# Kernel tuning notes

Hardware: AMD Instinct MI355X
Metric: run time of the kernel (lower is better)

## Reference

```python
import jax, jax.numpy as jnp
import numpy as np

B, L, D, H = 2, 2048, 1024, 16
HD = D // H


def _xavier(key, out_f, in_f):
    std = (2.0 / (in_f + out_f)) ** 0.5
    return jax.random.normal(key, (out_f, in_f), dtype=jnp.float32) * std


def setup_inputs() -> dict:
    key = jax.random.key(0)
    k = jax.random.split(key, 8)
    Q = jax.random.normal(k[0], (B, L, D), dtype=jnp.float32)
    K = jax.random.normal(k[1], (B, L, D), dtype=jnp.float32)
    V = jax.random.normal(k[2], (B, L, D), dtype=jnp.float32)
    mask = jnp.tril(jnp.ones((L, L), dtype=jnp.int32))[None, None]  # causal [1,1,L,L]
    wq = _xavier(k[3], D, D)
    wk = _xavier(k[4], D, D)
    wv = _xavier(k[5], D, D)
    wo = _xavier(k[6], D, D)
    bo = jnp.zeros((D,), dtype=jnp.float32)
    return {"Q": Q, "K": K, "V": V, "mask": mask,
            "wq": wq, "wk": wk, "wv": wv, "wo": wo, "bo": bo}


def reference(Q, K, V, mask, wq, wk, wv, wo, bo):
    N, Lq, Dm = Q.shape
    # projections: X @ W^T (Linear stores [out, in])
    q = (Q @ wq.T).reshape(N, Lq, H, HD).transpose(0, 2, 1, 3)  # [N,H,L,hd]
    kk = (K @ wk.T).reshape(N, Lq, H, HD).transpose(0, 2, 1, 3)
    v = (V @ wv.T).reshape(N, Lq, H, HD).transpose(0, 2, 1, 3)
    score = jnp.einsum('bhqd,bhkd->bhqk', q, kk) / jnp.sqrt(jnp.float32(HD))
    score = jnp.where(mask == 0, -jnp.inf, score)
    weights = jax.nn.softmax(score, axis=-1)
    attn = jnp.einsum('bhqk,bhkd->bhqd', weights, v)
    out = attn.transpose(0, 2, 1, 3).reshape(N, Lq, Dm)
    return out @ wo.T + bo
```

## Files before the change

kernel.cpp:

```cpp
#include <hip/hip_runtime.h>
#include <hip/hip_bf16.h>


#define B_ 2
#define L_ 2048
#define D_ 1024
#define H_ 16
#define HD_ 64
#define NA_ ((size_t)B_ * L_ * D_)
#define NW_ ((size_t)D_ * D_)

typedef __attribute__((ext_vector_type(8))) short bf16x8;
typedef __attribute__((ext_vector_type(4))) float f32x4;
typedef __hip_bfloat16 bf16;

__device__ __forceinline__ void async_load16(const void* g, void* l) {
  __builtin_amdgcn_global_load_lds((const __attribute__((address_space(1))) void*)g,
                                   (__attribute__((address_space(3))) void*)l,
                                   16, 0, 0);
}

__global__ __launch_bounds__(256) void xcvt_kernel(const float* __restrict__ q,
                                                   const float* __restrict__ k,
                                                   const float* __restrict__ v,
                                                   const float* __restrict__ w0,
                                                   const float* __restrict__ w1,
                                                   const float* __restrict__ w2,
                                                   const float* __restrict__ w3,
                                                   bf16* __restrict__ dst) {
  const int y = blockIdx.y;
  size_t i = ((size_t)blockIdx.x * 256 + threadIdx.x) * 4;
  const float* src;
  size_t soff = i;
  if (y < 3) {
    src = (y == 0) ? q : (y == 1) ? k : v;
  } else {
    int w = (int)(i >> 20);
    src = (w == 0) ? w0 : (w == 1) ? w1 : (w == 2) ? w2 : w3;
    soff = i & (NW_ - 1);
  }
  float4 vv = *(const float4*)(src + soff);
  union { bf16 h[4]; uint2 u; } pk;
  pk.h[0] = __float2bfloat16(vv.x);
  pk.h[1] = __float2bfloat16(vv.y);
  pk.h[2] = __float2bfloat16(vv.z);
  pk.h[3] = __float2bfloat16(vv.w);
  *(uint2*)(dst + (size_t)y * NA_ + i) = pk.u;
}

#define TS_ 136
__global__ __launch_bounds__(256) void gemm_qkv(const bf16* __restrict__ Qb,
                                                const bf16* __restrict__ Kb,
                                                const bf16* __restrict__ Vb,
                                                const bf16* __restrict__ Wb,
                                                bf16* __restrict__ qp,
                                                bf16* __restrict__ kp,
                                                bf16* __restrict__ vtp) {
  __shared__ __align__(16) bf16 smem[128 * TS_];
  bf16* As = smem;
  bf16* Bs = smem + 128 * 32;
  const int tid = threadIdx.x;
  const int wv = tid >> 6, lane = tid & 63;
  const int quad = lane >> 4, l16 = lane & 15;
  const int wm = wv & 1, wn = wv >> 1;
  const int m0 = blockIdx.x * 128, n0 = blockIdx.y * 128;
  const int z = blockIdx.z;
  const bf16* X = (z == 0) ? Qb : (z == 1) ? Kb : Vb;
  const bf16* W = Wb + (size_t)z * NW_;

  f32x4 acc[4][4];
#pragma unroll
  for (int i = 0; i < 4; i++)
#pragma unroll
    for (int j = 0; j < 4; j++) acc[i][j] = (f32x4){0.f, 0.f, 0.f, 0.f};

  for (int k0 = 0; k0 < D_; k0 += 32) {
#pragma unroll
    for (int it = 0; it < 2; it++) {
      int c = (wv * 2 + it) * 64 + lane;
      int row = c >> 2, cc = c & 3;
      async_load16(X + (size_t)(m0 + row) * D_ + k0 + cc * 8, (char*)As + c * 16);
      async_load16(W + (size_t)(n0 + row) * D_ + k0 + cc * 8, (char*)Bs + c * 16);
    }
    __syncthreads();
    bf16x8 af[4], bfr[4];
#pragma unroll
    for (int mi = 0; mi < 4; mi++)
      af[mi] = *(const bf16x8*)&As[(wm * 64 + mi * 16 + l16) * 32 + quad * 8];
#pragma unroll
    for (int ni = 0; ni < 4; ni++)
      bfr[ni] = *(const bf16x8*)&Bs[(wn * 64 + ni * 16 + l16) * 32 + quad * 8];
#pragma unroll
    for (int mi = 0; mi < 4; mi++)
#pragma unroll
      for (int ni = 0; ni < 4; ni++)
        acc[mi][ni] = __builtin_amdgcn_mfma_f32_16x16x32_bf16(af[mi], bfr[ni],
                                                              acc[mi][ni], 0, 0, 0);
    __syncthreads();
  }

  if (z == 2) {
    bf16* T = smem;
#pragma unroll
    for (int mi = 0; mi < 4; mi++) {
#pragma unroll
      for (int ni = 0; ni < 4; ni++) {
        int n_loc = wn * 64 + ni * 16 + l16;
        int m_loc = wm * 64 + mi * 16 + quad * 4;
        union { bf16 hx[4]; uint2 d; } pk;
#pragma unroll
        for (int r = 0; r < 4; r++) pk.hx[r] = __float2bfloat16(acc[mi][ni][r]);
        *(uint2*)&T[n_loc * TS_ + m_loc] = pk.d;
      }
    }
    __syncthreads();
#pragma unroll
    for (int p = 0; p < 8; p++) {
      int n_loc = p * 16 + (tid >> 4);
      int m_loc = (tid & 15) * 8;
      bf16x8 vv = *(const bf16x8*)&T[n_loc * TS_ + m_loc];
      int n = n0 + n_loc;
      int m = m0 + m_loc;
      int bb = m >> 11, l = m & (L_ - 1);
      int hh = n >> 6, hd = n & 63;
      *(bf16x8*)&vtp[((size_t)((bb * H_ + hh) * HD_ + hd)) * L_ + l] = vv;
    }
  } else {
    const float sc = (z == 0) ? 0.125f : 1.0f;
    bf16* dst = (z == 0) ? qp : kp;
#pragma unroll
    for (int mi = 0; mi < 4; mi++) {
#pragma unroll
      for (int ni = 0; ni < 4; ni++) {
        int n = n0 + wn * 64 + ni * 16 + l16;
#pragma unroll
        for (int r = 0; r < 4; r++) {
          int m = m0 + wm * 64 + mi * 16 + quad * 4 + r;
          dst[(size_t)m * D_ + n] = __float2bfloat16(acc[mi][ni][r] * sc);
        }
      }
    }
  }
}

__global__ __launch_bounds__(256) void attn_kernel(const bf16* __restrict__ qp,
                                                   const bf16* __restrict__ kp,
                                                   const bf16* __restrict__ vt,
                                                   bf16* __restrict__ attn) {
  __shared__ __align__(16) bf16 Kt[2][64 * 64];
  __shared__ __align__(16) bf16 Vt[2][64 * 64];
  __shared__ __align__(16) bf16 Pl[4][16 * 72];
  __shared__ __align__(16) bf16 Ph[4][16 * 72];
  const int tid = threadIdx.x;
  const int wv = tid >> 6, lane = tid & 63;
  const int quad = lane >> 4, l16 = lane & 15;
  const int pair = blockIdx.x, h = blockIdx.y, b = blockIdx.z;
  const int qlo = pair, qhi = (L_ / 64 - 1) - pair;

  const int rL = qlo * 64 + wv * 16 + l16;
  const int rH = qhi * 64 + wv * 16 + l16;
  bf16x8 qaL[2], qaH[2];
#pragma unroll
  for (int kk = 0; kk < 2; kk++) {
    qaL[kk] = *(const bf16x8*)&qp[((size_t)(b * L_ + rL)) * D_ + h * HD_ +
                                  kk * 32 + quad * 8];
    qaH[kk] = *(const bf16x8*)&qp[((size_t)(b * L_ + rH)) * D_ + h * HD_ +
                                  kk * 32 + quad * 8];
  }

  f32x4 OL[4], OH[4];
#pragma unroll
  for (int t = 0; t < 4; t++) {
    OL[t] = (f32x4){0.f, 0.f, 0.f, 0.f};
    OH[t] = (f32x4){0.f, 0.f, 0.f, 0.f};
  }
  float lL[4] = {0.f, 0.f, 0.f, 0.f}, lH[4] = {0.f, 0.f, 0.f, 0.f};

  const int csw = quad ^ (l16 & 7);

  auto stage = [&](int j, int buf) {
    const int j0 = j * 64;
#pragma unroll
    for (int it = 0; it < 2; it++) {
      int slot = (wv * 2 + it) * 64 + lane;
      int row = slot >> 3, c = (slot & 7) ^ (row & 7);
      async_load16(kp + ((size_t)(b * L_ + j0 + row)) * D_ + h * HD_ + c * 8,
                   (char*)Kt[buf] + slot * 16);
      async_load16(vt + ((size_t)((b * H_ + h) * HD_ + row)) * L_ + j0 + c * 8,
                   (char*)Vt[buf] + slot * 16);
    }
  };

  stage(0, 0);
  for (int j = 0; j <= qhi; j++) {
    const int buf = j & 1;
    const int j0 = j * 64;
    const bool doLo = (j <= qlo);
    __syncthreads();
    if (j < qhi) stage(j + 1, buf ^ 1);

    f32x4 sL[4], sH[4];
#pragma unroll
    for (int ss = 0; ss < 4; ss++) {
      int krow = ss * 16 + l16;
      bf16x8 kb0 = *(const bf16x8*)&Kt[buf][krow * 64 + csw * 8];
      bf16x8 kb1 = *(const bf16x8*)&Kt[buf][krow * 64 + (csw ^ 4) * 8];
      f32x4 s = (f32x4){0.f, 0.f, 0.f, 0.f};
      s = __builtin_amdgcn_mfma_f32_16x16x32_bf16(qaH[0], kb0, s, 0, 0, 0);
      s = __builtin_amdgcn_mfma_f32_16x16x32_bf16(qaH[1], kb1, s, 0, 0, 0);
      sH[ss] = s;
      if (doLo) {
        f32x4 t = (f32x4){0.f, 0.f, 0.f, 0.f};
        t = __builtin_amdgcn_mfma_f32_16x16x32_bf16(qaL[0], kb0, t, 0, 0, 0);
        t = __builtin_amdgcn_mfma_f32_16x16x32_bf16(qaL[1], kb1, t, 0, 0, 0);
        sL[ss] = t;
      }
    }

    if (j == qhi) {
#pragma unroll
      for (int ss = 0; ss < 4; ss++) {
        int key = j0 + ss * 16 + l16;
#pragma unroll
        for (int r = 0; r < 4; r++) {
          int rq = qhi * 64 + wv * 16 + quad * 4 + r;
          if (key > rq) sH[ss][r] = -1e30f;
        }
      }
    }
    if (doLo && j == qlo) {
#pragma unroll
      for (int ss = 0; ss < 4; ss++) {
        int key = j0 + ss * 16 + l16;
#pragma unroll
        for (int r = 0; r < 4; r++) {
          int rq = qlo * 64 + wv * 16 + quad * 4 + r;
          if (key > rq) sL[ss][r] = -1e30f;
        }
      }
    }
#pragma unroll
    for (int ss = 0; ss < 4; ss++) {
#pragma unroll
      for (int r = 0; r < 4; r++) {
        float p = __expf(sH[ss][r]);
        lH[r] += p;
        Ph[wv][(quad * 4 + r) * 72 + ss * 16 + l16] = __float2bfloat16(p);
      }
    }
    if (doLo) {
#pragma unroll
      for (int ss = 0; ss < 4; ss++) {
#pragma unroll
        for (int r = 0; r < 4; r++) {
          float p = __expf(sL[ss][r]);
          lL[r] += p;
          Pl[wv][(quad * 4 + r) * 72 + ss * 16 + l16] = __float2bfloat16(p);
        }
      }
    }

    asm volatile("s_waitcnt lgkmcnt(0)" ::: "memory");

#pragma unroll
    for (int kk = 0; kk < 2; kk++) {
      bf16x8 pah = *(const bf16x8*)&Ph[wv][l16 * 72 + kk * 32 + quad * 8];
      bf16x8 pal;
      if (doLo) pal = *(const bf16x8*)&Pl[wv][l16 * 72 + kk * 32 + quad * 8];
#pragma unroll
      for (int t = 0; t < 4; t++) {
        bf16x8 vb = *(const bf16x8*)&Vt[buf][(t * 16 + l16) * 64 + (csw ^ (kk * 4)) * 8];
        OH[t] = __builtin_amdgcn_mfma_f32_16x16x32_bf16(pah, vb, OH[t], 0, 0, 0);
        if (doLo) OL[t] = __builtin_amdgcn_mfma_f32_16x16x32_bf16(pal, vb, OL[t], 0, 0, 0);
      }
    }
  }

#pragma unroll
  for (int r = 0; r < 4; r++) {
#pragma unroll
    for (int off = 1; off < 16; off <<= 1) {
      lL[r] += __shfl_xor(lL[r], off, 64);
      lH[r] += __shfl_xor(lH[r], off, 64);
    }
  }
#pragma unroll
  for (int t = 0; t < 4; t++) {
#pragma unroll
    for (int r = 0; r < 4; r++) {
      int rowL = qlo * 64 + wv * 16 + quad * 4 + r;
      int rowH = qhi * 64 + wv * 16 + quad * 4 + r;
      attn[((size_t)(b * L_ + rowL)) * D_ + h * HD_ + t * 16 + l16] =
          __float2bfloat16(OL[t][r] / lL[r]);
      attn[((size_t)(b * L_ + rowH)) * D_ + h * HD_ + t * 16 + l16] =
          __float2bfloat16(OH[t][r] / lH[r]);
    }
  }
}

__global__ __launch_bounds__(256) void gemm_out(const bf16* __restrict__ X,
                                                const bf16* __restrict__ W,
                                                const float* __restrict__ bias,
                                                float* __restrict__ out) {
  __shared__ __align__(16) bf16 As[64 * 32];
  __shared__ __align__(16) bf16 Bs[128 * 32];
  const int tid = threadIdx.x;
  const int wv = tid >> 6, lane = tid & 63;
  const int quad = lane >> 4, l16 = lane & 15;
  const int wm = wv & 1, wn = wv >> 1;
  const int m0 = blockIdx.x * 64, n0 = blockIdx.y * 128;

  f32x4 acc[2][4];
#pragma unroll
  for (int i = 0; i < 2; i++)
#pragma unroll
    for (int j = 0; j < 4; j++) acc[i][j] = (f32x4){0.f, 0.f, 0.f, 0.f};

  for (int k0 = 0; k0 < D_; k0 += 32) {
    {
      int c = tid;
      int row = c >> 2, cc = c & 3;
      async_load16(X + (size_t)(m0 + row) * D_ + k0 + cc * 8, (char*)As + c * 16);
    }
#pragma unroll
    for (int it = 0; it < 2; it++) {
      int c = (wv * 2 + it) * 64 + lane;
      int row = c >> 2, cc = c & 3;
      async_load16(W + (size_t)(n0 + row) * D_ + k0 + cc * 8, (char*)Bs + c * 16);
    }
    __syncthreads();
    bf16x8 af[2], bfr[4];
#pragma unroll
    for (int mi = 0; mi < 2; mi++)
      af[mi] = *(const bf16x8*)&As[(wm * 32 + mi * 16 + l16) * 32 + quad * 8];
#pragma unroll
    for (int ni = 0; ni < 4; ni++)
      bfr[ni] = *(const bf16x8*)&Bs[(wn * 64 + ni * 16 + l16) * 32 + quad * 8];
#pragma unroll
    for (int mi = 0; mi < 2; mi++)
#pragma unroll
      for (int ni = 0; ni < 4; ni++)
        acc[mi][ni] = __builtin_amdgcn_mfma_f32_16x16x32_bf16(af[mi], bfr[ni],
                                                              acc[mi][ni], 0, 0, 0);
    __syncthreads();
  }

#pragma unroll
  for (int mi = 0; mi < 2; mi++) {
#pragma unroll
    for (int ni = 0; ni < 4; ni++) {
      int n = n0 + wn * 64 + ni * 16 + l16;
      float bval = bias[n];
#pragma unroll
      for (int r = 0; r < 4; r++) {
        int m = m0 + wm * 32 + mi * 16 + quad * 4 + r;
        out[(size_t)m * D_ + n] = acc[mi][ni][r] + bval;
      }
    }
  }
}

extern "C" void kernel_launch(void* const* d_in, const int* in_sizes, int n_in,
                              void* d_out, int out_size, void* d_ws, size_t ws_size,
                              hipStream_t stream) {
  const float* Q  = (const float*)d_in[0];
  const float* K  = (const float*)d_in[1];
  const float* V  = (const float*)d_in[2];
  const float* wq = (const float*)d_in[4];
  const float* wk = (const float*)d_in[5];
  const float* wvp = (const float*)d_in[6];
  const float* wo = (const float*)d_in[7];
  const float* bo = (const float*)d_in[8];
  float* out = (float*)d_out;

  bf16* base = (bf16*)d_ws;
  bf16* Qb = base;
  bf16* Kb = Qb + NA_;
  bf16* Vb = Kb + NA_;
  bf16* Wb = Vb + NA_;
  bf16* qp = Wb + 4 * NW_;
  bf16* kp = qp + NA_;
  bf16* vt = kp + NA_;
  bf16* at = vt + NA_;

  xcvt_kernel<<<dim3(NA_ / 1024, 4), 256, 0, stream>>>(Q, K, V, wq, wk, wvp, wo, base);
  gemm_qkv<<<dim3(32, 8, 3), 256, 0, stream>>>(Qb, Kb, Vb, Wb, qp, kp, vt);
  attn_kernel<<<dim3(L_ / 128, H_, B_), 256, 0, stream>>>(qp, kp, vt, at);
  gemm_out<<<dim3(64, 8), 256, 0, stream>>>(at, Wb + 3 * NW_, bo, out);
}
```

Baseline: 232.1 us.

## Swizzle GEMM block order per XCD and transpose attention score MFMA layout

Both GEMM kernels remap the linear block id so that consecutive ids sent round-robin to the 8 XCDs handle neighbouring tiles, improving L2 reuse of the A/B panels. In the attention kernel the score MFMA operands are swapped, so each lane holds 4 consecutive keys for a single query row. This lets P be written to LDS as one packed 8-byte store instead of four scalar bf16 stores, and the row sum becomes one scalar per lane, cutting the end-of-kernel shuffle reduction. s_setprio is raised around the MFMA phases to favour matrix issue across waves. The changes risk subtle mask and indexing mistakes, and the remap assumes exact grid sizes.

```diff
diff --git a/kernel.cpp b/kernel.cpp
--- a/kernel.cpp
+++ b/kernel.cpp
@@ -63,8 +63,10 @@
   const int wv = tid >> 6, lane = tid & 63;
   const int quad = lane >> 4, l16 = lane & 15;
   const int wm = wv & 1, wn = wv >> 1;
-  const int m0 = blockIdx.x * 128, n0 = blockIdx.y * 128;
-  const int z = blockIdx.z;
+  const int id = blockIdx.x + 32 * blockIdx.y + 256 * blockIdx.z;
+  const int swz = (id & 7) * 96 + (id >> 3);
+  const int m0 = (swz & 31) * 128, n0 = ((swz >> 5) & 7) * 128;
+  const int z = swz >> 8;
   const bf16* X = (z == 0) ? Qb : (z == 1) ? Kb : Vb;
   const bf16* W = Wb + (size_t)z * NW_;
 
@@ -157,14 +159,14 @@
   const int pair = blockIdx.x, h = blockIdx.y, b = blockIdx.z;
   const int qlo = pair, qhi = (L_ / 64 - 1) - pair;
 
-  const int rL = qlo * 64 + wv * 16 + l16;
-  const int rH = qhi * 64 + wv * 16 + l16;
+  const int rLq = qlo * 64 + wv * 16 + l16;
+  const int rHq = qhi * 64 + wv * 16 + l16;
   bf16x8 qaL[2], qaH[2];
 #pragma unroll
   for (int kk = 0; kk < 2; kk++) {
-    qaL[kk] = *(const bf16x8*)&qp[((size_t)(b * L_ + rL)) * D_ + h * HD_ +
+    qaL[kk] = *(const bf16x8*)&qp[((size_t)(b * L_ + rLq)) * D_ + h * HD_ +
                                   kk * 32 + quad * 8];
-    qaH[kk] = *(const bf16x8*)&qp[((size_t)(b * L_ + rH)) * D_ + h * HD_ +
+    qaH[kk] = *(const bf16x8*)&qp[((size_t)(b * L_ + rHq)) * D_ + h * HD_ +
                                   kk * 32 + quad * 8];
   }
 
@@ -174,7 +176,7 @@
     OL[t] = (f32x4){0.f, 0.f, 0.f, 0.f};
     OH[t] = (f32x4){0.f, 0.f, 0.f, 0.f};
   }
-  float lL[4] = {0.f, 0.f, 0.f, 0.f}, lH[4] = {0.f, 0.f, 0.f, 0.f};
+  float lL = 0.f, lH = 0.f;
 
   const int csw = quad ^ (l16 & 7);
 
@@ -200,68 +202,74 @@
     if (j < qhi) stage(j + 1, buf ^ 1);
 
     f32x4 sL[4], sH[4];
+    __builtin_amdgcn_s_setprio(1);
 #pragma unroll
     for (int ss = 0; ss < 4; ss++) {
       int krow = ss * 16 + l16;
       bf16x8 kb0 = *(const bf16x8*)&Kt[buf][krow * 64 + csw * 8];
       bf16x8 kb1 = *(const bf16x8*)&Kt[buf][krow * 64 + (csw ^ 4) * 8];
-      f32x4 s = (f32x4){0.f, 0.f, 0.f, 0.f};
-      s = __builtin_amdgcn_mfma_f32_16x16x32_bf16(qaH[0], kb0, s, 0, 0, 0);
-      s = __builtin_amdgcn_mfma_f32_16x16x32_bf16(qaH[1], kb1, s, 0, 0, 0);
-      sH[ss] = s;
+      f32x4 t = (f32x4){0.f, 0.f, 0.f, 0.f};
+      t = __builtin_amdgcn_mfma_f32_16x16x32_bf16(kb0, qaH[0], t, 0, 0, 0);
+      t = __builtin_amdgcn_mfma_f32_16x16x32_bf16(kb1, qaH[1], t, 0, 0, 0);
+      sH[ss] = t;
       if (doLo) {
-        f32x4 t = (f32x4){0.f, 0.f, 0.f, 0.f};
-        t = __builtin_amdgcn_mfma_f32_16x16x32_bf16(qaL[0], kb0, t, 0, 0, 0);
-        t = __builtin_amdgcn_mfma_f32_16x16x32_bf16(qaL[1], kb1, t, 0, 0, 0);
-        sL[ss] = t;
-      }
-    }
+        f32x4 u = (f32x4){0.f, 0.f, 0.f, 0.f};
+        u = __builtin_amdgcn_mfma_f32_16x16x32_bf16(kb0, qaL[0], u, 0, 0, 0);
+        u = __builtin_amdgcn_mfma_f32_16x16x32_bf16(kb1, qaL[1], u, 0, 0, 0);
+        sL[ss] = u;
+      }
+    }
+    __builtin_amdgcn_s_setprio(0);
 
     if (j == qhi) {
 #pragma unroll
+      for (int ss = 0; ss < 4; ss++)
+#pragma unroll
+        for (int r = 0; r < 4; r++) {
+          int key = j0 + ss * 16 + quad * 4 + r;
+          if (key > rHq) sH[ss][r] = -1e30f;
+        }
+    }
+    if (doLo && j == qlo) {
+#pragma unroll
+      for (int ss = 0; ss < 4; ss++)
+#pragma unroll
+        for (int r = 0; r < 4; r++) {
+          int key = j0 + ss * 16 + quad * 4 + r;
+          if (key > rLq) sL[ss][r] = -1e30f;
+        }
+    }
+
+#pragma unroll
+    for (int ss = 0; ss < 4; ss++) {
+      float p0 = __expf(sH[ss][0]), p1 = __expf(sH[ss][1]);
+      float p2 = __expf(sH[ss][2]), p3 = __expf(sH[ss][3]);
+      lH += (p0 + p1) + (p2 + p3);
+      union { bf16 hx[4]; uint2 d; } pk;
+      pk.hx[0] = __float2bfloat16(p0);
+      pk.hx[1] = __float2bfloat16(p1);
+      pk.hx[2] = __float2bfloat16(p2);
+      pk.hx[3] = __float2bfloat16(p3);
+      *(uint2*)&Ph[wv][l16 * 72 + ss * 16 + quad * 4] = pk.d;
+    }
+    if (doLo) {
+#pragma unroll
       for (int ss = 0; ss < 4; ss++) {
-        int key = j0 + ss * 16 + l16;
-#pragma unroll
-        for (int r = 0; r < 4; r++) {
-          int rq = qhi * 64 + wv * 16 + quad * 4 + r;
-          if (key > rq) sH[ss][r] = -1e30f;
-        }
-      }
-    }
-    if (doLo && j == qlo) {
-#pragma unroll
-      for (int ss = 0; ss < 4; ss++) {
-        int key = j0 + ss * 16 + l16;
-#pragma unroll
-        for (int r = 0; r < 4; r++) {
-          int rq = qlo * 64 + wv * 16 + quad * 4 + r;
-          if (key > rq) sL[ss][r] = -1e30f;
-        }
-      }
-    }
-#pragma unroll
-    for (int ss = 0; ss < 4; ss++) {
-#pragma unroll
-      for (int r = 0; r < 4; r++) {
-        float p = __expf(sH[ss][r]);
-        lH[r] += p;
-        Ph[wv][(quad * 4 + r) * 72 + ss * 16 + l16] = __float2bfloat16(p);
-      }
-    }
-    if (doLo) {
-#pragma unroll
-      for (int ss = 0; ss < 4; ss++) {
-#pragma unroll
-        for (int r = 0; r < 4; r++) {
-          float p = __expf(sL[ss][r]);
-          lL[r] += p;
-          Pl[wv][(quad * 4 + r) * 72 + ss * 16 + l16] = __float2bfloat16(p);
-        }
+        float p0 = __expf(sL[ss][0]), p1 = __expf(sL[ss][1]);
+        float p2 = __expf(sL[ss][2]), p3 = __expf(sL[ss][3]);
+        lL += (p0 + p1) + (p2 + p3);
+        union { bf16 hx[4]; uint2 d; } pk;
+        pk.hx[0] = __float2bfloat16(p0);
+        pk.hx[1] = __float2bfloat16(p1);
+        pk.hx[2] = __float2bfloat16(p2);
+        pk.hx[3] = __float2bfloat16(p3);
+        *(uint2*)&Pl[wv][l16 * 72 + ss * 16 + quad * 4] = pk.d;
       }
     }
 
     asm volatile("s_waitcnt lgkmcnt(0)" ::: "memory");
 
+    __builtin_amdgcn_s_setprio(1);
 #pragma unroll
     for (int kk = 0; kk < 2; kk++) {
       bf16x8 pah = *(const bf16x8*)&Ph[wv][l16 * 72 + kk * 32 + quad * 8];
@@ -274,16 +282,20 @@
         if (doLo) OL[t] = __builtin_amdgcn_mfma_f32_16x16x32_bf16(pal, vb, OL[t], 0, 0, 0);
       }
     }
-  }
-
+    __builtin_amdgcn_s_setprio(0);
+  }
+
+  lL += __shfl_xor(lL, 16, 64);
+  lL += __shfl_xor(lL, 32, 64);
+  lH += __shfl_xor(lH, 16, 64);
+  lH += __shfl_xor(lH, 32, 64);
+  float lLq[4], lHq[4];
 #pragma unroll
   for (int r = 0; r < 4; r++) {
-#pragma unroll
-    for (int off = 1; off < 16; off <<= 1) {
-      lL[r] += __shfl_xor(lL[r], off, 64);
-      lH[r] += __shfl_xor(lH[r], off, 64);
-    }
-  }
+    lLq[r] = __shfl(lL, quad * 4 + r, 64);
+    lHq[r] = __shfl(lH, quad * 4 + r, 64);
+  }
+
 #pragma unroll
   for (int t = 0; t < 4; t++) {
 #pragma unroll
@@ -291,9 +303,9 @@
       int rowL = qlo * 64 + wv * 16 + quad * 4 + r;
       int rowH = qhi * 64 + wv * 16 + quad * 4 + r;
       attn[((size_t)(b * L_ + rowL)) * D_ + h * HD_ + t * 16 + l16] =
-          __float2bfloat16(OL[t][r] / lL[r]);
+          __float2bfloat16(OL[t][r] / lLq[r]);
       attn[((size_t)(b * L_ + rowH)) * D_ + h * HD_ + t * 16 + l16] =
-          __float2bfloat16(OH[t][r] / lH[r]);
+          __float2bfloat16(OH[t][r] / lHq[r]);
     }
   }
 }
@@ -308,7 +320,9 @@
   const int wv = tid >> 6, lane = tid & 63;
   const int quad = lane >> 4, l16 = lane & 15;
   const int wm = wv & 1, wn = wv >> 1;
-  const int m0 = blockIdx.x * 64, n0 = blockIdx.y * 128;
+  const int id = blockIdx.x + 64 * blockIdx.y;
+  const int swz = (id & 7) * 64 + (id >> 3);
+  const int m0 = (swz & 63) * 64, n0 = (swz >> 6) * 128;
 
   f32x4 acc[2][4];
 #pragma unroll
```

Result: no change. 228.8 us (-1.4%).
